# Kernel optimization log

Hardware: AMD Instinct MI355X
Metric: run time of the kernel (lower is better)

The kernel has to match this reference:

```python
import jax, jax.numpy as jnp
import numpy as np

THRE = 4.0  # ReLUX threshold / multispike lens
EPS = 1e-5  # BatchNorm eps (torch default)

@jax.custom_vjp
def spike(x):
    # multispike forward: floor(clamp(x,0,4)+0.5)
    return jnp.floor(jnp.clip(x, 0.0, THRE) + 0.5)

def _spike_fwd(x):
    return spike(x), x

def _spike_bwd(x, g):
    # surrogate gradient: pass-through on 0 < x < lens
    return (g * ((x > 0) & (x < THRE)).astype(g.dtype),)

spike.defvjp(_spike_fwd, _spike_bwd)


def setup_inputs() -> dict:
    key = jax.random.key(0)
    k0, k1, k2 = jax.random.split(key, 3)
    B, N, C = 4, 1024, 512
    x = jax.random.normal(k0, (B, N, C), jnp.float32)
    Wqkv = jax.random.normal(k1, (3 * C, C), jnp.float32) * (C ** -0.5)  # Linear weight [out,in], no bias
    gamma = jnp.ones((3 * C,), jnp.float32)   # BN weight
    beta = jnp.zeros((3 * C,), jnp.float32)   # BN bias
    Wproj = jax.random.normal(k2, (C, C), jnp.float32) * (C ** -0.5)
    bproj = jnp.zeros((C,), jnp.float32)
    return {"x": x, "Wqkv": Wqkv, "gamma": gamma, "beta": beta, "Wproj": Wproj, "bproj": bproj}


def reference(x, Wqkv, gamma, beta, Wproj, bproj):
    B, N, C = x.shape
    H = 8
    hd = C // H
    scale = hd ** -0.5

    xs = spike(x)                                    # head_spike
    qkv = jnp.einsum('bnc,dc->bnd', xs, Wqkv)        # [B,N,3C]
    # BatchNorm1d over channel dim with batch stats across (B, N)
    mu = qkv.mean(axis=(0, 1))
    var = qkv.var(axis=(0, 1))
    qkv = (qkv - mu) * jax.lax.rsqrt(var + EPS) * gamma + beta

    qkv = qkv.reshape(B, N, 3, H, hd).transpose(2, 0, 3, 1, 4)  # [3,B,H,N,hd]
    q = spike(qkv[0])
    k = spike(qkv[1])
    v = spike(qkv[2])

    attn = jnp.einsum('bhnd,bhmd->bhnm', q, k)       # no softmax
    attn = spike(attn)
    out = jnp.einsum('bhnm,bhmd->bhnd', attn, v) * scale
    out = out.transpose(0, 2, 1, 3).reshape(B, N, C)
    out = spike(out)                                 # project_spike
    return jnp.einsum('bnc,dc->bnd', out, Wproj) + bproj
```

## Files before the change

kernel.cpp:

```cpp
#include <hip/hip_runtime.h>

typedef __attribute__((ext_vector_type(8))) short short8;
typedef __attribute__((ext_vector_type(4))) short short4v;
typedef __attribute__((ext_vector_type(8))) signed char s8x8;
typedef __attribute__((ext_vector_type(4))) unsigned char u8x4;
typedef __attribute__((ext_vector_type(4))) float f32x4;
typedef __attribute__((ext_vector_type(4))) int int4v;
typedef __attribute__((ext_vector_type(4))) unsigned int u32x4;

#define THRE 4.0f

#define GLOAD_LDS16(g, l) \
    __builtin_amdgcn_global_load_lds((const __attribute__((address_space(1))) void*)(g), \
                                     (__attribute__((address_space(3))) void*)(l), 16, 0, 0)

__device__ __forceinline__ float spikef(float x) {
    return floorf(fminf(fmaxf(x, 0.0f), THRE) + 0.5f);
}
__device__ __forceinline__ unsigned short f2bf(float f) {
    return (unsigned short)(__builtin_bit_cast(unsigned int, f) >> 16);
}
__device__ __forceinline__ unsigned short f2bf_rn(float f) {
    unsigned u = __builtin_bit_cast(unsigned int, f);
    unsigned r = ((u >> 16) & 1u) + 0x7FFFu;
    return (unsigned short)((u + r) >> 16);
}
__device__ __forceinline__ float bf2f(unsigned short s) {
    return __builtin_bit_cast(float, (unsigned int)s << 16);
}
__device__ __forceinline__ int4v mfma_i8(u32x4 a, u32x4 b, int4v c) {
    return __builtin_amdgcn_mfma_i32_16x16x64_i8(__builtin_bit_cast(int4v, a),
                                                 __builtin_bit_cast(int4v, b), c, 0, 0, 0);
}

__global__ void k_prep(const float* __restrict__ x,
                       const float* __restrict__ Wq, const float* __restrict__ Wp,
                       unsigned char* __restrict__ xs8, signed char* __restrict__ Wq8,
                       float* __restrict__ wscale, short* __restrict__ Wpd) {
    const int blk = blockIdx.x, tid = threadIdx.x;
    if (blk < 2048) {
        const int i = blk * 256 + tid;
        const float4 v = *(const float4*)&x[(size_t)i * 4];
        u8x4 o;
        o.x = (unsigned char)spikef(v.x);
        o.y = (unsigned char)spikef(v.y);
        o.z = (unsigned char)spikef(v.z);
        o.w = (unsigned char)spikef(v.w);
        *(u8x4*)&xs8[(size_t)i * 4] = o;
    } else if (blk < 2432) {
        const int row = (blk - 2048) * 4 + (tid >> 6);
        const int lane = tid & 63;
        const float* wr = Wq + (size_t)row * 512 + lane * 8;
        float w[8];
        float mx = 0.f;
        #pragma unroll
        for (int i = 0; i < 8; ++i) { w[i] = wr[i]; mx = fmaxf(mx, fabsf(w[i])); }
        #pragma unroll
        for (int o = 32; o > 0; o >>= 1) mx = fmaxf(mx, __shfl_xor(mx, o, 64));
        const float inv = mx > 0.f ? 127.0f / mx : 0.f;
        s8x8 q;
        #pragma unroll
        for (int i = 0; i < 8; ++i) q[i] = (signed char)rintf(w[i] * inv);
        *(s8x8*)&Wq8[(size_t)row * 512 + lane * 8] = q;
        if (lane == 0) wscale[row] = mx > 0.f ? mx / 127.0f : 0.f;
    } else {
        const int i = (blk - 2432) * 256 + tid;
        const float4 v = *(const float4*)&Wp[(size_t)i * 4];
        short4v o;
        o.x = (short)f2bf_rn(v.x);
        o.y = (short)f2bf_rn(v.y);
        o.z = (short)f2bf_rn(v.z);
        o.w = (short)f2bf_rn(v.w);
        *(short4v*)&Wpd[(size_t)i * 4] = o;
    }
}

__global__ __launch_bounds__(256) void k_gemm_qkv(const unsigned char* __restrict__ A,
                                                  const signed char* __restrict__ B,
                                                  const float* __restrict__ wscale,
                                                  short* __restrict__ C,
                                                  float* __restrict__ psum,
                                                  float* __restrict__ psq) {
    __shared__ __align__(16) unsigned char As[128 * 128];
    __shared__ __align__(16) unsigned char Bs[96 * 128];
    const int tid  = threadIdx.x;
    const int lane = tid & 63, wv = tid >> 6;
    const int wy = wv >> 1, wx = wv & 1;
    const int quad = lane >> 4, l16 = lane & 15;
    const int u = blockIdx.x;
    const int mtile = u & 31;
    const int m0 = mtile * 128, n0 = (u >> 5) * 96;
    const int N = 1536;

    int4v acc[4][3];
    #pragma unroll
    for (int i = 0; i < 4; ++i)
        #pragma unroll
        for (int j = 0; j < 3; ++j)
            #pragma unroll
            for (int r = 0; r < 4; ++r) acc[i][j][r] = 0;

    const unsigned char* gA[4]; unsigned char* lA[4];
    #pragma unroll
    for (int i = 0; i < 4; ++i) {
        int L = wv + 4 * i;
        int c = L * 64 + lane;
        int r = c >> 3, g = (c & 7) ^ (r & 7);
        gA[i] = A + (size_t)(m0 + r) * 512 + g * 16;
        lA[i] = &As[(size_t)c * 16];
    }
    const unsigned char* gB[3]; unsigned char* lB[3];
    #pragma unroll
    for (int i = 0; i < 3; ++i) {
        int L = wv + 4 * i;
        int c = L * 64 + lane;
        int r = c >> 3, g = (c & 7) ^ (r & 7);
        gB[i] = (const unsigned char*)B + (size_t)(n0 + r) * 512 + g * 16;
        lB[i] = &Bs[(size_t)c * 16];
    }

    for (int k0 = 0; k0 < 512; k0 += 128) {
        __syncthreads();
        #pragma unroll
        for (int i = 0; i < 4; ++i) GLOAD_LDS16(gA[i] + k0, lA[i]);
        #pragma unroll
        for (int i = 0; i < 3; ++i) GLOAD_LDS16(gB[i] + k0, lB[i]);
        __syncthreads();
        #pragma unroll
        for (int kk = 0; kk < 2; ++kk) {
            u32x4 aF[4], bF[3];
            #pragma unroll
            for (int mt = 0; mt < 4; ++mt) {
                const int r = wy * 64 + mt * 16 + l16;
                aF[mt] = *(const u32x4*)&As[(size_t)r * 128 + (((kk * 4 + quad) ^ (r & 7)) * 16)];
            }
            #pragma unroll
            for (int nt = 0; nt < 3; ++nt) {
                const int r = wx * 48 + nt * 16 + l16;
                bF[nt] = *(const u32x4*)&Bs[(size_t)r * 128 + (((kk * 4 + quad) ^ (r & 7)) * 16)];
            }
            #pragma unroll
            for (int mt = 0; mt < 4; ++mt)
                #pragma unroll
                for (int nt = 0; nt < 3; ++nt)
                    acc[mt][nt] = mfma_i8(aF[mt], bF[nt], acc[mt][nt]);
        }
    }

    float sc[3];
    #pragma unroll
    for (int nt = 0; nt < 3; ++nt) sc[nt] = wscale[n0 + wx * 48 + nt * 16 + l16];

    float vacc[4][3][4];
    #pragma unroll
    for (int mt = 0; mt < 4; ++mt)
        #pragma unroll
        for (int r = 0; r < 4; ++r) {
            int row = m0 + wy * 64 + mt * 16 + quad * 4 + r;
            short* Cr = C + (size_t)row * N + n0 + wx * 48 + l16;
            #pragma unroll
            for (int nt = 0; nt < 3; ++nt) {
                float v = (float)acc[mt][nt][r] * sc[nt];
                vacc[mt][nt][r] = v;
                Cr[nt * 16] = (short)f2bf_rn(v);
            }
        }

    __syncthreads();
    float* PS = (float*)As;
    float* PQ = (float*)Bs;
    #pragma unroll
    for (int nt = 0; nt < 3; ++nt) {
        float s = 0.f, q = 0.f;
        #pragma unroll
        for (int mt = 0; mt < 4; ++mt)
            #pragma unroll
            for (int r = 0; r < 4; ++r) {
                float v = vacc[mt][nt][r];
                s += v;
                q = fmaf(v, v, q);
            }
        PS[(wy * 4 + quad) * 96 + wx * 48 + nt * 16 + l16] = s;
        PQ[(wy * 4 + quad) * 96 + wx * 48 + nt * 16 + l16] = q;
    }
    __syncthreads();
    if (tid < 96) {
        float s = 0.f, q = 0.f;
        #pragma unroll
        for (int i = 0; i < 8; ++i) { s += PS[i * 96 + tid]; q += PQ[i * 96 + tid]; }
        psum[mtile * 1536 + n0 + tid] = s;
        psq [mtile * 1536 + n0 + tid] = q;
    }
}

__global__ __launch_bounds__(256) void k_gemm_proj(const short* __restrict__ A,
                                                   const short* __restrict__ B,
                                                   const float* __restrict__ bias,
                                                   float* __restrict__ C) {
    __shared__ __align__(16) short As[32 * 64];
    __shared__ __align__(16) short Bs[128 * 64];
    const int tid  = threadIdx.x;
    const int lane = tid & 63, wv = tid >> 6;
    const int wy = wv >> 1, wx = wv & 1;
    const int quad = lane >> 4, l16 = lane & 15;
    const int u = blockIdx.x;
    const int mtile = u & 127;
    const int m0 = mtile * 32, n0 = (u >> 7) * 128;
    const int K = 512, N = 512;

    f32x4 acc[4];
    #pragma unroll
    for (int j = 0; j < 4; ++j)
        #pragma unroll
        for (int r = 0; r < 4; ++r) acc[j][r] = 0.f;

    const short* gA0; short* lA0;
    {
        int c = tid;
        int r = c >> 3, g = (c & 7) ^ (r & 7);
        gA0 = A + (size_t)(m0 + r) * K + g * 8;
        lA0 = &As[(size_t)c * 8];
    }
    const short* gB[4]; short* lB[4];
    #pragma unroll
    for (int i = 0; i < 4; ++i) {
        int c = tid + 256 * i;
        int r = c >> 3, g = (c & 7) ^ (r & 7);
        gB[i] = B + (size_t)(n0 + r) * K + g * 8;
        lB[i] = &Bs[(size_t)c * 8];
    }

    for (int k0 = 0; k0 < K; k0 += 64) {
        __syncthreads();
        GLOAD_LDS16(gA0 + k0, lA0);
        #pragma unroll
        for (int i = 0; i < 4; ++i) GLOAD_LDS16(gB[i] + k0, lB[i]);
        __syncthreads();
        #pragma unroll
        for (int kk = 0; kk < 2; ++kk) {
            const int ra = wy * 16 + l16;
            short8 aF = *(const short8*)&As[(size_t)ra * 64 + (((kk * 4 + quad) ^ (ra & 7)) * 8)];
            #pragma unroll
            for (int nt = 0; nt < 4; ++nt) {
                const int rb = wx * 64 + nt * 16 + l16;
                short8 bF = *(const short8*)&Bs[(size_t)rb * 64 + (((kk * 4 + quad) ^ (rb & 7)) * 8)];
                acc[nt] = __builtin_amdgcn_mfma_f32_16x16x32_bf16(aF, bF, acc[nt], 0, 0, 0);
            }
        }
    }

    float bs[4];
    #pragma unroll
    for (int nt = 0; nt < 4; ++nt) bs[nt] = bias[n0 + wx * 64 + nt * 16 + l16];
    #pragma unroll
    for (int r = 0; r < 4; ++r) {
        int row = m0 + wy * 16 + quad * 4 + r;
        float* Cr = C + (size_t)row * N + n0 + wx * 64 + l16;
        #pragma unroll
        for (int nt = 0; nt < 4; ++nt) Cr[nt * 16] = acc[nt][r] + bs[nt];
    }
}

__global__ __launch_bounds__(256) void k_bn_spike(const short* __restrict__ qkvb,
                           const float* __restrict__ psum, const float* __restrict__ psq,
                           const float* __restrict__ gamma, const float* __restrict__ beta,
                           unsigned char* __restrict__ qp, unsigned char* __restrict__ kp,
                           unsigned char* __restrict__ vt) {
    __shared__ float sa[64], sb[64];
    __shared__ __align__(16) unsigned char tile[64 * 80];
    const int tid = threadIdx.x;
    const int slice = blockIdx.x;
    const int c0 = slice * 64;
    const int r0 = blockIdx.y * 256;
    const int b = r0 >> 10, nb = r0 & 1023;

    if (tid < 64) {
        const int c = c0 + tid;
        double s = 0.0, q = 0.0;
        for (int st = 0; st < 32; ++st) { s += (double)psum[st * 1536 + c]; q += (double)psq[st * 1536 + c]; }
        const double mu  = s / 4096.0;
        const double var = q / 4096.0 - mu * mu;
        const float a = (float)((double)gamma[c] / sqrt(var + 1e-5));
        sa[tid] = a;
        sb[tid] = fmaf(-(float)mu, a, beta[c]);
    }
    __syncthreads();

    if (slice < 16) {
        const int h = slice & 7;
        const int ch4 = (tid & 15) * 4, rr = tid >> 4;
        const float4 A4 = *(const float4*)&sa[ch4];
        const float4 B4 = *(const float4*)&sb[ch4];
        unsigned char* base = (slice < 8 ? qp : kp) + (((size_t)b * 8 + h) * 1024 + nb) * 64;
        for (int i = rr; i < 256; i += 16) {
            const short4v v4 = *(const short4v*)&qkvb[(size_t)(r0 + i) * 1536 + c0 + ch4];
            u8x4 o;
            o.x = (unsigned char)spikef(fmaf(bf2f((unsigned short)v4.x), A4.x, B4.x));
            o.y = (unsigned char)spikef(fmaf(bf2f((unsigned short)v4.y), A4.y, B4.y));
            o.z = (unsigned char)spikef(fmaf(bf2f((unsigned short)v4.z), A4.z, B4.z));
            o.w = (unsigned char)spikef(fmaf(bf2f((unsigned short)v4.w), A4.w, B4.w));
            *(u8x4*)&base[(size_t)i * 64 + ch4] = o;
        }
    } else {
        const int h = slice - 16;
        const int ch = tid & 63, rq = tid >> 6;
        const float A = sa[ch], Bsh = sb[ch];
        const int e = tid >> 2, j0 = (tid & 3) * 16;
        unsigned char* vbase = vt + (size_t)b * 524288 + (size_t)h * 65536
                             + (size_t)(nb >> 8) * 16384 + e * 64 + j0;
        for (int rb = 0; rb < 4; ++rb) {
            __syncthreads();
            for (int i = rq; i < 64; i += 4) {
                float v = bf2f((unsigned short)qkvb[(size_t)(r0 + rb * 64 + i) * 1536 + c0 + ch]);
                tile[ch * 80 + i] = (unsigned char)spikef(fmaf(v, A, Bsh));
            }
            __syncthreads();
            *(u32x4*)&vbase[rb * 4096] = *(const u32x4*)&tile[e * 80 + j0];
        }
    }
}

__global__ __launch_bounds__(256) void k_attn(const unsigned char* __restrict__ qp,
                                              const unsigned char* __restrict__ kp,
                                              const unsigned char* __restrict__ vt,
                                              short* __restrict__ sout) {
    __shared__ __align__(16) unsigned int Sb[2][64 * 68];
    const int tid  = threadIdx.x;
    const int lane = tid & 63, w = tid >> 6;
    const int quad = lane >> 4, l16 = lane & 15;
    const int u = blockIdx.x;
    const int bhid = u & 31;
    const int b = bhid >> 3, h = bhid & 7;
    const int n0 = (u >> 5) * 64;
    const size_t bh = (size_t)b * 8 + h;

    const unsigned char* Kb = kp + bh * 65536;
    const unsigned char* Vb = vt + bh * 65536;

    u32x4 qf[4];
    #pragma unroll
    for (int mt = 0; mt < 4; ++mt)
        qf[mt] = *(const u32x4*)&qp[(bh * 1024 + n0 + mt * 16 + l16) * 64 + quad * 16];

    int4v of[4];
    #pragma unroll
    for (int mt = 0; mt < 4; ++mt)
        #pragma unroll
        for (int r = 0; r < 4; ++r) of[mt][r] = 0;

    u32x4 kfc[4];
    #pragma unroll
    for (int jt = 0; jt < 4; ++jt)
        kfc[jt] = *(const u32x4*)&Kb[(size_t)(w * 64 + jt * 16 + l16) * 64 + quad * 16];

    #pragma unroll
    for (int t = 0; t < 4; ++t) {
        u32x4 bV[4];
        #pragma unroll
        for (int kk = 0; kk < 4; ++kk)
            bV[kk] = *(const u32x4*)&Vb[(size_t)((t * 4 + kk) * 64 + w * 16 + l16) * 64 + quad * 16];

        __builtin_amdgcn_s_setprio(1);
        #pragma unroll
        for (int jt = 0; jt < 4; ++jt) {
            #pragma unroll
            for (int mt = 0; mt < 4; ++mt) {
                int4v z;
                #pragma unroll
                for (int r = 0; r < 4; ++r) z[r] = 0;
                int4v s = mfma_i8(kfc[jt], qf[mt], z);
                unsigned int pkk = 0;
                #pragma unroll
                for (int r = 0; r < 4; ++r) {
                    int v = s[r]; v = v < 0 ? 0 : (v > 4 ? 4 : v);
                    pkk |= (unsigned int)v << (8 * r);
                }
                Sb[t & 1][(mt * 16 + l16) * 68 + w * 16 + jt * 4 + quad] = pkk;
            }
        }
        __builtin_amdgcn_s_setprio(0);
        __syncthreads();

        if (t < 3) {
            #pragma unroll
            for (int jt = 0; jt < 4; ++jt)
                kfc[jt] = *(const u32x4*)&Kb[(size_t)((t + 1) * 256 + w * 64 + jt * 16 + l16) * 64 + quad * 16];
        }

        __builtin_amdgcn_s_setprio(1);
        #pragma unroll
        for (int kk = 0; kk < 4; ++kk) {
            #pragma unroll
            for (int mt = 0; mt < 4; ++mt) {
                u32x4 aS = *(const u32x4*)&Sb[t & 1][(mt * 16 + l16) * 68 + kk * 16 + quad * 4];
                of[mt] = mfma_i8(aS, bV[kk], of[mt]);
            }
        }
        __builtin_amdgcn_s_setprio(0);
    }

    #pragma unroll
    for (int mt = 0; mt < 4; ++mt)
        #pragma unroll
        for (int r = 0; r < 4; ++r) {
            size_t orow = (size_t)b * 1024 + n0 + mt * 16 + quad * 4 + r;
            sout[orow * 512 + h * 64 + w * 16 + l16] =
                (short)f2bf(spikef((float)of[mt][r] * 0.125f));
        }
}

extern "C" void kernel_launch(void* const* d_in, const int* in_sizes, int n_in,
                              void* d_out, int out_size, void* d_ws, size_t ws_size,
                              hipStream_t stream) {
    const float* x     = (const float*)d_in[0];
    const float* Wqkv  = (const float*)d_in[1];
    const float* gamma = (const float*)d_in[2];
    const float* beta  = (const float*)d_in[3];
    const float* Wproj = (const float*)d_in[4];
    const float* bproj = (const float*)d_in[5];
    float* out = (float*)d_out;

    char* w = (char*)d_ws;
    unsigned char* xs8   = (unsigned char*)(w);
    signed char* Wq8     = (signed char*)(w + 8388608);
    float* wscale        = (float*)(w + 9437184);
    short* Wproj2        = (short*)(w + 11534336);
    short* qkvb          = (short*)(w + 12582912);
    unsigned char* qp    = (unsigned char*)(w + 37748736);
    unsigned char* kp    = (unsigned char*)(w + 41943040);
    unsigned char* vt    = (unsigned char*)(w + 46137344);
    float* psum          = (float*)(w + 50331648);
    float* psq           = psum + 32 * 1536;
    short* sout          = (short*)(w);

    k_prep<<<2688, 256, 0, stream>>>(x, Wqkv, Wproj, xs8, Wq8, wscale, Wproj2);
    k_gemm_qkv<<<512, 256, 0, stream>>>(xs8, Wq8, wscale, qkvb, psum, psq);
    k_bn_spike<<<dim3(24, 16), 256, 0, stream>>>(qkvb, psum, psq, gamma, beta, qp, kp, vt);
    k_attn<<<512, 256, 0, stream>>>(qp, kp, vt, sout);
    k_gemm_proj<<<512, 256, 0, stream>>>(sout, Wproj2, bproj, out);
}
```

Baseline: 108.9 us.

## Fuse prep into QKV GEMM and BN-spike into attention kernel

Removes the separate prep and BN-spike kernels. The QKV GEMM now reads fp32 x and Wqkv directly, spiking and quantizing them to int8 while filling LDS, with per-row weight scales computed in the block prologue. The attention kernel applies the BatchNorm affine and spike to bf16 q/k/v on the fly, transposes V through LDS, and also converts Wproj to bf16. This saves two launches and the int8 intermediate round-trips. In exchange, x and W are re-read and re-quantized by every tile that uses them, global_load_lds async copies become synchronous register loads, and the strided per-column V gathers in attention may be uncoalesced.

New measurement: 204.2 us. 1.87x slower.

```diff
diff --git a/kernel.cpp b/kernel.cpp
--- a/kernel.cpp
+++ b/kernel.cpp
@@ -2,8 +2,6 @@
 
 typedef __attribute__((ext_vector_type(8))) short short8;
 typedef __attribute__((ext_vector_type(4))) short short4v;
-typedef __attribute__((ext_vector_type(8))) signed char s8x8;
-typedef __attribute__((ext_vector_type(4))) unsigned char u8x4;
 typedef __attribute__((ext_vector_type(4))) float f32x4;
 typedef __attribute__((ext_vector_type(4))) int int4v;
 typedef __attribute__((ext_vector_type(4))) unsigned int u32x4;
@@ -33,56 +31,14 @@
                                                  __builtin_bit_cast(int4v, b), c, 0, 0, 0);
 }
 
-__global__ void k_prep(const float* __restrict__ x,
-                       const float* __restrict__ Wq, const float* __restrict__ Wp,
-                       unsigned char* __restrict__ xs8, signed char* __restrict__ Wq8,
-                       float* __restrict__ wscale, short* __restrict__ Wpd) {
-    const int blk = blockIdx.x, tid = threadIdx.x;
-    if (blk < 2048) {
-        const int i = blk * 256 + tid;
-        const float4 v = *(const float4*)&x[(size_t)i * 4];
-        u8x4 o;
-        o.x = (unsigned char)spikef(v.x);
-        o.y = (unsigned char)spikef(v.y);
-        o.z = (unsigned char)spikef(v.z);
-        o.w = (unsigned char)spikef(v.w);
-        *(u8x4*)&xs8[(size_t)i * 4] = o;
-    } else if (blk < 2432) {
-        const int row = (blk - 2048) * 4 + (tid >> 6);
-        const int lane = tid & 63;
-        const float* wr = Wq + (size_t)row * 512 + lane * 8;
-        float w[8];
-        float mx = 0.f;
-        #pragma unroll
-        for (int i = 0; i < 8; ++i) { w[i] = wr[i]; mx = fmaxf(mx, fabsf(w[i])); }
-        #pragma unroll
-        for (int o = 32; o > 0; o >>= 1) mx = fmaxf(mx, __shfl_xor(mx, o, 64));
-        const float inv = mx > 0.f ? 127.0f / mx : 0.f;
-        s8x8 q;
-        #pragma unroll
-        for (int i = 0; i < 8; ++i) q[i] = (signed char)rintf(w[i] * inv);
-        *(s8x8*)&Wq8[(size_t)row * 512 + lane * 8] = q;
-        if (lane == 0) wscale[row] = mx > 0.f ? mx / 127.0f : 0.f;
-    } else {
-        const int i = (blk - 2432) * 256 + tid;
-        const float4 v = *(const float4*)&Wp[(size_t)i * 4];
-        short4v o;
-        o.x = (short)f2bf_rn(v.x);
-        o.y = (short)f2bf_rn(v.y);
-        o.z = (short)f2bf_rn(v.z);
-        o.w = (short)f2bf_rn(v.w);
-        *(short4v*)&Wpd[(size_t)i * 4] = o;
-    }
-}
-
-__global__ __launch_bounds__(256) void k_gemm_qkv(const unsigned char* __restrict__ A,
-                                                  const signed char* __restrict__ B,
-                                                  const float* __restrict__ wscale,
-                                                  short* __restrict__ C,
-                                                  float* __restrict__ psum,
-                                                  float* __restrict__ psq) {
+__global__ __launch_bounds__(256) void k_qkv(const float* __restrict__ x,
+                                             const float* __restrict__ Wq,
+                                             short* __restrict__ C,
+                                             float* __restrict__ psum,
+                                             float* __restrict__ psq) {
     __shared__ __align__(16) unsigned char As[128 * 128];
     __shared__ __align__(16) unsigned char Bs[96 * 128];
+    __shared__ float invB[96], scB[96];
     const int tid  = threadIdx.x;
     const int lane = tid & 63, wv = tid >> 6;
     const int wy = wv >> 1, wx = wv & 1;
@@ -92,6 +48,27 @@
     const int m0 = mtile * 128, n0 = (u >> 5) * 96;
     const int N = 1536;
 
+    #pragma unroll
+    for (int rr = 0; rr < 3; ++rr) {
+        const int row = rr * 32 + (tid >> 3);
+        const int ln8 = tid & 7;
+        const float* wr = Wq + (size_t)(n0 + row) * 512 + ln8 * 64;
+        float mx = 0.f;
+        #pragma unroll
+        for (int i = 0; i < 16; ++i) {
+            const float4 f = *(const float4*)(wr + i * 4);
+            mx = fmaxf(mx, fmaxf(fmaxf(fabsf(f.x), fabsf(f.y)), fmaxf(fabsf(f.z), fabsf(f.w))));
+        }
+        mx = fmaxf(mx, __shfl_xor(mx, 1, 64));
+        mx = fmaxf(mx, __shfl_xor(mx, 2, 64));
+        mx = fmaxf(mx, __shfl_xor(mx, 4, 64));
+        if (ln8 == 0) {
+            invB[row] = mx > 0.f ? 127.0f / mx : 0.f;
+            scB[row]  = mx > 0.f ? mx / 127.0f : 0.f;
+        }
+    }
+    __syncthreads();
+
     int4v acc[4][3];
     #pragma unroll
     for (int i = 0; i < 4; ++i)
@@ -100,31 +77,43 @@
             #pragma unroll
             for (int r = 0; r < 4; ++r) acc[i][j][r] = 0;
 
-    const unsigned char* gA[4]; unsigned char* lA[4];
-    #pragma unroll
-    for (int i = 0; i < 4; ++i) {
-        int L = wv + 4 * i;
-        int c = L * 64 + lane;
-        int r = c >> 3, g = (c & 7) ^ (r & 7);
-        gA[i] = A + (size_t)(m0 + r) * 512 + g * 16;
-        lA[i] = &As[(size_t)c * 16];
-    }
-    const unsigned char* gB[3]; unsigned char* lB[3];
-    #pragma unroll
-    for (int i = 0; i < 3; ++i) {
-        int L = wv + 4 * i;
-        int c = L * 64 + lane;
-        int r = c >> 3, g = (c & 7) ^ (r & 7);
-        gB[i] = (const unsigned char*)B + (size_t)(n0 + r) * 512 + g * 16;
-        lB[i] = &Bs[(size_t)c * 16];
-    }
-
     for (int k0 = 0; k0 < 512; k0 += 128) {
         __syncthreads();
         #pragma unroll
-        for (int i = 0; i < 4; ++i) GLOAD_LDS16(gA[i] + k0, lA[i]);
-        #pragma unroll
-        for (int i = 0; i < 3; ++i) GLOAD_LDS16(gB[i] + k0, lB[i]);
+        for (int i = 0; i < 4; ++i) {
+            const int c = (wv + 4 * i) * 64 + lane;
+            const int r = c >> 3, g = (c & 7) ^ (r & 7);
+            const float* src = x + (size_t)(m0 + r) * 512 + k0 + g * 16;
+            u32x4 ov;
+            #pragma unroll
+            for (int d = 0; d < 4; ++d) {
+                const float4 f = *(const float4*)(src + d * 4);
+                unsigned dw  = (unsigned)(unsigned char)spikef(f.x);
+                dw |= (unsigned)(unsigned char)spikef(f.y) << 8;
+                dw |= (unsigned)(unsigned char)spikef(f.z) << 16;
+                dw |= (unsigned)(unsigned char)spikef(f.w) << 24;
+                ov[d] = dw;
+            }
+            *(u32x4*)&As[(size_t)c * 16] = ov;
+        }
+        #pragma unroll
+        for (int i = 0; i < 3; ++i) {
+            const int c = (wv + 4 * i) * 64 + lane;
+            const int r = c >> 3, g = (c & 7) ^ (r & 7);
+            const float* src = Wq + (size_t)(n0 + r) * 512 + k0 + g * 16;
+            const float inv = invB[r];
+            u32x4 ov;
+            #pragma unroll
+            for (int d = 0; d < 4; ++d) {
+                const float4 f = *(const float4*)(src + d * 4);
+                unsigned dw  = ((unsigned)(int)rintf(f.x * inv)) & 255u;
+                dw |= (((unsigned)(int)rintf(f.y * inv)) & 255u) << 8;
+                dw |= (((unsigned)(int)rintf(f.z * inv)) & 255u) << 16;
+                dw |= (((unsigned)(int)rintf(f.w * inv)) & 255u) << 24;
+                ov[d] = dw;
+            }
+            *(u32x4*)&Bs[(size_t)c * 16] = ov;
+        }
         __syncthreads();
         #pragma unroll
         for (int kk = 0; kk < 2; ++kk) {
@@ -149,7 +138,7 @@
 
     float sc[3];
     #pragma unroll
-    for (int nt = 0; nt < 3; ++nt) sc[nt] = wscale[n0 + wx * 48 + nt * 16 + l16];
+    for (int nt = 0; nt < 3; ++nt) sc[nt] = scB[wx * 48 + nt * 16 + l16];
 
     float vacc[4][3][4];
     #pragma unroll
@@ -191,6 +180,168 @@
         psum[mtile * 1536 + n0 + tid] = s;
         psq [mtile * 1536 + n0 + tid] = q;
     }
+}
+
+__global__ __launch_bounds__(256) void k_attn2(const short* __restrict__ qkvb,
+                                               const float* __restrict__ psum,
+                                               const float* __restrict__ psq,
+                                               const float* __restrict__ gamma,
+                                               const float* __restrict__ beta,
+                                               const float* __restrict__ Wp,
+                                               short* __restrict__ Wpd,
+                                               short* __restrict__ sout) {
+    __shared__ __align__(16) float sa[192], sb[192];
+    __shared__ __align__(16) unsigned char Vt[64 * 272];
+    __shared__ __align__(16) unsigned int Sbuf[64 * 68];
+    const int tid  = threadIdx.x;
+    const int lane = tid & 63, wv = tid >> 6;
+    const int quad = lane >> 4, l16 = lane & 15;
+    const int u = blockIdx.x;
+    const int bhid = u & 31;
+    const int b = bhid >> 3, h = bhid & 7;
+    const int n0 = (u >> 5) * 64;
+    const size_t qrow_base = (size_t)b * 1024;
+
+    {
+        const int i = u * 256 + tid;
+        const float2 f = *(const float2*)&Wp[(size_t)i * 2];
+        ((unsigned*)Wpd)[i] = (unsigned)f2bf_rn(f.x) | ((unsigned)f2bf_rn(f.y) << 16);
+    }
+
+    if (tid < 192) {
+        const int g = tid >> 6, cc = tid & 63;
+        const int c = g * 512 + h * 64 + cc;
+        double s = 0.0, q = 0.0;
+        for (int st = 0; st < 32; ++st) { s += (double)psum[st * 1536 + c]; q += (double)psq[st * 1536 + c]; }
+        const double mu  = s / 4096.0;
+        const double var = q / 4096.0 - mu * mu;
+        const float a = (float)((double)gamma[c] / sqrt(var + 1e-5));
+        sa[tid] = a;
+        sb[tid] = fmaf(-(float)mu, a, beta[c]);
+    }
+    __syncthreads();
+
+    f32x4 aQ[4], bQ[4], aK[4], bK[4];
+    #pragma unroll
+    for (int d = 0; d < 4; ++d) {
+        aQ[d] = *(const f32x4*)&sa[quad * 16 + d * 4];
+        bQ[d] = *(const f32x4*)&sb[quad * 16 + d * 4];
+        aK[d] = *(const f32x4*)&sa[64 + quad * 16 + d * 4];
+        bK[d] = *(const f32x4*)&sb[64 + quad * 16 + d * 4];
+    }
+    const int vch = tid >> 2;
+    const int vj0 = (tid & 3) * 4;
+    const float aV = sa[128 + vch], bV0 = sb[128 + vch];
+    const short* vsrc = qkvb + 1024 + h * 64 + vch;
+
+    u32x4 qf[4];
+    #pragma unroll
+    for (int mt = 0; mt < 4; ++mt) {
+        const short* src = qkvb + (qrow_base + n0 + mt * 16 + l16) * 1536 + h * 64 + quad * 16;
+        const short8 v0 = *(const short8*)src;
+        const short8 v1 = *(const short8*)(src + 8);
+        u32x4 r;
+        #pragma unroll
+        for (int d = 0; d < 4; ++d) {
+            unsigned dw = 0;
+            #pragma unroll
+            for (int j = 0; j < 4; ++j) {
+                const int idx = d * 4 + j;
+                const float f = bf2f((unsigned short)(idx < 8 ? v0[idx] : v1[idx - 8]));
+                dw |= (unsigned)(unsigned char)spikef(fmaf(f, aQ[d][j], bQ[d][j])) << (8 * j);
+            }
+            r[d] = dw;
+        }
+        qf[mt] = r;
+    }
+
+    int4v of[4];
+    #pragma unroll
+    for (int mt = 0; mt < 4; ++mt)
+        #pragma unroll
+        for (int r = 0; r < 4; ++r) of[mt][r] = 0;
+
+    for (int t = 0; t < 4; ++t) {
+        __syncthreads();
+        {
+            const short* bt = vsrc + (qrow_base + t * 256) * 1536;
+            #pragma unroll
+            for (int k = 0; k < 16; ++k) {
+                unsigned dw = 0;
+                #pragma unroll
+                for (int i = 0; i < 4; ++i) {
+                    const int j = vj0 + k * 16 + i;
+                    const float f = bf2f((unsigned short)bt[(size_t)j * 1536]);
+                    dw |= (unsigned)(unsigned char)spikef(fmaf(f, aV, bV0)) << (8 * i);
+                }
+                *(unsigned*)&Vt[vch * 272 + vj0 + k * 16] = dw;
+            }
+        }
+        u32x4 kf[4];
+        #pragma unroll
+        for (int jt = 0; jt < 4; ++jt) {
+            const short* src = qkvb + (qrow_base + t * 256 + wv * 64 + jt * 16 + l16) * 1536
+                             + 512 + h * 64 + quad * 16;
+            const short8 v0 = *(const short8*)src;
+            const short8 v1 = *(const short8*)(src + 8);
+            u32x4 r;
+            #pragma unroll
+            for (int d = 0; d < 4; ++d) {
+                unsigned dw = 0;
+                #pragma unroll
+                for (int j = 0; j < 4; ++j) {
+                    const int idx = d * 4 + j;
+                    const float f = bf2f((unsigned short)(idx < 8 ? v0[idx] : v1[idx - 8]));
+                    dw |= (unsigned)(unsigned char)spikef(fmaf(f, aK[d][j], bK[d][j])) << (8 * j);
+                }
+                r[d] = dw;
+            }
+            kf[jt] = r;
+        }
+        __syncthreads();
+
+        __builtin_amdgcn_s_setprio(1);
+        #pragma unroll
+        for (int jt = 0; jt < 4; ++jt) {
+            #pragma unroll
+            for (int mt = 0; mt < 4; ++mt) {
+                int4v z;
+                #pragma unroll
+                for (int r = 0; r < 4; ++r) z[r] = 0;
+                int4v s = mfma_i8(kf[jt], qf[mt], z);
+                unsigned pkk = 0;
+                #pragma unroll
+                for (int r = 0; r < 4; ++r) {
+                    int v = s[r]; v = v < 0 ? 0 : (v > 4 ? 4 : v);
+                    pkk |= (unsigned)v << (8 * r);
+                }
+                Sbuf[(mt * 16 + l16) * 68 + wv * 16 + jt * 4 + quad] = pkk;
+            }
+        }
+        __builtin_amdgcn_s_setprio(0);
+        __syncthreads();
+
+        __builtin_amdgcn_s_setprio(1);
+        #pragma unroll
+        for (int kk = 0; kk < 4; ++kk) {
+            const u32x4 bVf = *(const u32x4*)&Vt[(wv * 16 + l16) * 272 + (kk * 4 + quad) * 16];
+            #pragma unroll
+            for (int mt = 0; mt < 4; ++mt) {
+                const u32x4 aS = *(const u32x4*)&Sbuf[(mt * 16 + l16) * 68 + kk * 16 + quad * 4];
+                of[mt] = mfma_i8(aS, bVf, of[mt]);
+            }
+        }
+        __builtin_amdgcn_s_setprio(0);
+    }
+
+    #pragma unroll
+    for (int mt = 0; mt < 4; ++mt)
+        #pragma unroll
+        for (int r = 0; r < 4; ++r) {
+            size_t orow = qrow_base + n0 + mt * 16 + quad * 4 + r;
+            sout[orow * 512 + h * 64 + wv * 16 + l16] =
+                (short)f2bf(spikef((float)of[mt][r] * 0.125f));
+        }
 }
 
 __global__ __launch_bounds__(256) void k_gemm_proj(const short* __restrict__ A,
@@ -261,154 +412,6 @@
     }
 }
 
-__global__ __launch_bounds__(256) void k_bn_spike(const short* __restrict__ qkvb,
-                           const float* __restrict__ psum, const float* __restrict__ psq,
-                           const float* __restrict__ gamma, const float* __restrict__ beta,
-                           unsigned char* __restrict__ qp, unsigned char* __restrict__ kp,
-                           unsigned char* __restrict__ vt) {
-    __shared__ float sa[64], sb[64];
-    __shared__ __align__(16) unsigned char tile[64 * 80];
-    const int tid = threadIdx.x;
-    const int slice = blockIdx.x;
-    const int c0 = slice * 64;
-    const int r0 = blockIdx.y * 256;
-    const int b = r0 >> 10, nb = r0 & 1023;
-
-    if (tid < 64) {
-        const int c = c0 + tid;
-        double s = 0.0, q = 0.0;
-        for (int st = 0; st < 32; ++st) { s += (double)psum[st * 1536 + c]; q += (double)psq[st * 1536 + c]; }
-        const double mu  = s / 4096.0;
-        const double var = q / 4096.0 - mu * mu;
-        const float a = (float)((double)gamma[c] / sqrt(var + 1e-5));
-        sa[tid] = a;
-        sb[tid] = fmaf(-(float)mu, a, beta[c]);
-    }
-    __syncthreads();
-
-    if (slice < 16) {
-        const int h = slice & 7;
-        const int ch4 = (tid & 15) * 4, rr = tid >> 4;
-        const float4 A4 = *(const float4*)&sa[ch4];
-        const float4 B4 = *(const float4*)&sb[ch4];
-        unsigned char* base = (slice < 8 ? qp : kp) + (((size_t)b * 8 + h) * 1024 + nb) * 64;
-        for (int i = rr; i < 256; i += 16) {
-            const short4v v4 = *(const short4v*)&qkvb[(size_t)(r0 + i) * 1536 + c0 + ch4];
-            u8x4 o;
-            o.x = (unsigned char)spikef(fmaf(bf2f((unsigned short)v4.x), A4.x, B4.x));
-            o.y = (unsigned char)spikef(fmaf(bf2f((unsigned short)v4.y), A4.y, B4.y));
-            o.z = (unsigned char)spikef(fmaf(bf2f((unsigned short)v4.z), A4.z, B4.z));
-            o.w = (unsigned char)spikef(fmaf(bf2f((unsigned short)v4.w), A4.w, B4.w));
-            *(u8x4*)&base[(size_t)i * 64 + ch4] = o;
-        }
-    } else {
-        const int h = slice - 16;
-        const int ch = tid & 63, rq = tid >> 6;
-        const float A = sa[ch], Bsh = sb[ch];
-        const int e = tid >> 2, j0 = (tid & 3) * 16;
-        unsigned char* vbase = vt + (size_t)b * 524288 + (size_t)h * 65536
-                             + (size_t)(nb >> 8) * 16384 + e * 64 + j0;
-        for (int rb = 0; rb < 4; ++rb) {
-            __syncthreads();
-            for (int i = rq; i < 64; i += 4) {
-                float v = bf2f((unsigned short)qkvb[(size_t)(r0 + rb * 64 + i) * 1536 + c0 + ch]);
-                tile[ch * 80 + i] = (unsigned char)spikef(fmaf(v, A, Bsh));
-            }
-            __syncthreads();
-            *(u32x4*)&vbase[rb * 4096] = *(const u32x4*)&tile[e * 80 + j0];
-        }
-    }
-}
-
-__global__ __launch_bounds__(256) void k_attn(const unsigned char* __restrict__ qp,
-                                              const unsigned char* __restrict__ kp,
-                                              const unsigned char* __restrict__ vt,
-                                              short* __restrict__ sout) {
-    __shared__ __align__(16) unsigned int Sb[2][64 * 68];
-    const int tid  = threadIdx.x;
-    const int lane = tid & 63, w = tid >> 6;
-    const int quad = lane >> 4, l16 = lane & 15;
-    const int u = blockIdx.x;
-    const int bhid = u & 31;
-    const int b = bhid >> 3, h = bhid & 7;
-    const int n0 = (u >> 5) * 64;
-    const size_t bh = (size_t)b * 8 + h;
-
-    const unsigned char* Kb = kp + bh * 65536;
-    const unsigned char* Vb = vt + bh * 65536;
-
-    u32x4 qf[4];
-    #pragma unroll
-    for (int mt = 0; mt < 4; ++mt)
-        qf[mt] = *(const u32x4*)&qp[(bh * 1024 + n0 + mt * 16 + l16) * 64 + quad * 16];
-
-    int4v of[4];
-    #pragma unroll
-    for (int mt = 0; mt < 4; ++mt)
-        #pragma unroll
-        for (int r = 0; r < 4; ++r) of[mt][r] = 0;
-
-    u32x4 kfc[4];
-    #pragma unroll
-    for (int jt = 0; jt < 4; ++jt)
-        kfc[jt] = *(const u32x4*)&Kb[(size_t)(w * 64 + jt * 16 + l16) * 64 + quad * 16];
-
-    #pragma unroll
-    for (int t = 0; t < 4; ++t) {
-        u32x4 bV[4];
-        #pragma unroll
-        for (int kk = 0; kk < 4; ++kk)
-            bV[kk] = *(const u32x4*)&Vb[(size_t)((t * 4 + kk) * 64 + w * 16 + l16) * 64 + quad * 16];
-
-        __builtin_amdgcn_s_setprio(1);
-        #pragma unroll
-        for (int jt = 0; jt < 4; ++jt) {
-            #pragma unroll
-            for (int mt = 0; mt < 4; ++mt) {
-                int4v z;
-                #pragma unroll
-                for (int r = 0; r < 4; ++r) z[r] = 0;
-                int4v s = mfma_i8(kfc[jt], qf[mt], z);
-                unsigned int pkk = 0;
-                #pragma unroll
-                for (int r = 0; r < 4; ++r) {
-                    int v = s[r]; v = v < 0 ? 0 : (v > 4 ? 4 : v);
-                    pkk |= (unsigned int)v << (8 * r);
-                }
-                Sb[t & 1][(mt * 16 + l16) * 68 + w * 16 + jt * 4 + quad] = pkk;
-            }
-        }
-        __builtin_amdgcn_s_setprio(0);
-        __syncthreads();
-
-        if (t < 3) {
-            #pragma unroll
-            for (int jt = 0; jt < 4; ++jt)
-                kfc[jt] = *(const u32x4*)&Kb[(size_t)((t + 1) * 256 + w * 64 + jt * 16 + l16) * 64 + quad * 16];
-        }
-
-        __builtin_amdgcn_s_setprio(1);
-        #pragma unroll
-        for (int kk = 0; kk < 4; ++kk) {
-            #pragma unroll
-            for (int mt = 0; mt < 4; ++mt) {
-                u32x4 aS = *(const u32x4*)&Sb[t & 1][(mt * 16 + l16) * 68 + kk * 16 + quad * 4];
-                of[mt] = mfma_i8(aS, bV[kk], of[mt]);
-            }
-        }
-        __builtin_amdgcn_s_setprio(0);
-    }
-
-    #pragma unroll
-    for (int mt = 0; mt < 4; ++mt)
-        #pragma unroll
-        for (int r = 0; r < 4; ++r) {
-            size_t orow = (size_t)b * 1024 + n0 + mt * 16 + quad * 4 + r;
-            sout[orow * 512 + h * 64 + w * 16 + l16] =
-                (short)f2bf(spikef((float)of[mt][r] * 0.125f));
-        }
-}
-
 extern "C" void kernel_launch(void* const* d_in, const int* in_sizes, int n_in,
                               void* d_out, int out_size, void* d_ws, size_t ws_size,
                               hipStream_t stream) {
@@ -421,21 +424,13 @@
     float* out = (float*)d_out;
 
     char* w = (char*)d_ws;
-    unsigned char* xs8   = (unsigned char*)(w);
-    signed char* Wq8     = (signed char*)(w + 8388608);
-    float* wscale        = (float*)(w + 9437184);
-    short* Wproj2        = (short*)(w + 11534336);
+    short* Wpd           = (short*)(w + 11534336);
     short* qkvb          = (short*)(w + 12582912);
-    unsigned char* qp    = (unsigned char*)(w + 37748736);
-    unsigned char* kp    = (unsigned char*)(w + 41943040);
-    unsigned char* vt    = (unsigned char*)(w + 46137344);
     float* psum          = (float*)(w + 50331648);
     float* psq           = psum + 32 * 1536;
     short* sout          = (short*)(w);
 
-    k_prep<<<2688, 256, 0, stream>>>(x, Wqkv, Wproj, xs8, Wq8, wscale, Wproj2);
-    k_gemm_qkv<<<512, 256, 0, stream>>>(xs8, Wq8, wscale, qkvb, psum, psq);
-    k_bn_spike<<<dim3(24, 16), 256, 0, stream>>>(qkvb, psum, psq, gamma, beta, qp, kp, vt);
-    k_attn<<<512, 256, 0, stream>>>(qp, kp, vt, sout);
-    k_gemm_proj<<<512, 256, 0, stream>>>(sout, Wproj2, bproj, out);
-}
+    k_qkv  <<<512, 256, 0, stream>>>(x, Wqkv, qkvb, psum, psq);
+    k_attn2<<<512, 256, 0, stream>>>(qkvb, psum, psq, gamma, beta, Wproj, Wpd, sout);
+    k_gemm_proj<<<512, 256, 0, stream>>>(sout, Wpd, bproj, out);
+}
```
